# Performance work log

Measured on AMD Instinct MI355X. Metric: run time of the kernel, lower is better.

The kernel has to match this reference:

```python
import jax, jax.numpy as jnp
import numpy as np
import math

B, QLEN, DMODEL, NHEAD, SKV = 16, 1, 2048, 32, 4096
HEAD_DIM = DMODEL // NHEAD  # 64


def setup_inputs() -> dict:
    key = jax.random.key(0)
    ks = jax.random.split(key, 12)
    x = jax.random.normal(ks[0], (B, QLEN, DMODEL), dtype=jnp.float32)
    last_pos = jax.random.randint(ks[1], (B,), 0, SKV, dtype=jnp.int64)
    # mask: attend to cache positions <= last_pos (broadcast over heads and q)
    mask = (jnp.arange(SKV)[None, :] <= last_pos[:, None]).reshape(B, 1, 1, SKV)
    s = 1.0 / math.sqrt(DMODEL)
    Wq = jax.random.normal(ks[2], (DMODEL, DMODEL), dtype=jnp.float32) * s
    bq = jax.random.normal(ks[3], (DMODEL,), dtype=jnp.float32) * 0.02
    Wk = jax.random.normal(ks[4], (DMODEL, DMODEL), dtype=jnp.float32) * s
    bk = jax.random.normal(ks[5], (DMODEL,), dtype=jnp.float32) * 0.02
    Wv = jax.random.normal(ks[6], (DMODEL, DMODEL), dtype=jnp.float32) * s
    bv = jax.random.normal(ks[7], (DMODEL,), dtype=jnp.float32) * 0.02
    Wo = jax.random.normal(ks[8], (DMODEL, DMODEL), dtype=jnp.float32) * s
    bo = jax.random.normal(ks[9], (DMODEL,), dtype=jnp.float32) * 0.02
    # prefilled KV cache (float32, as in the module)
    cache_k = jax.random.normal(ks[10], (B, NHEAD, SKV, HEAD_DIM), dtype=jnp.float32)
    cache_v = jax.random.normal(ks[11], (B, NHEAD, SKV, HEAD_DIM), dtype=jnp.float32)
    return {"x": x, "last_pos": last_pos, "mask": mask, "Wq": Wq, "bq": bq,
            "Wk": Wk, "bk": bk, "Wv": Wv, "bv": bv, "Wo": Wo, "bo": bo,
            "cache_k": cache_k, "cache_v": cache_v}


def reference(x, last_pos, mask, Wq, bq, Wk, bk, Wv, bv, Wo, bo, cache_k, cache_v):
    bsz, seq_len, _ = x.shape  # decode path: seq_len == 1
    # QKV projections -> [B, H, S, D]
    q = (x @ Wq + bq).reshape(bsz, seq_len, NHEAD, HEAD_DIM).transpose(0, 2, 1, 3)
    k = (x @ Wk + bk).reshape(bsz, seq_len, NHEAD, HEAD_DIM).transpose(0, 2, 1, 3)
    v = (x @ Wv + bv).reshape(bsz, seq_len, NHEAD, HEAD_DIM).transpose(0, 2, 1, 3)
    # KV-cache scatter update at last_pos (seq_len == 1 branch of the original)
    bidx = jnp.arange(bsz)
    updated_kcache = cache_k.at[bidx, :, last_pos, :].set(k[:, :, 0, :].astype(jnp.float32))
    updated_vcache = cache_v.at[bidx, :, last_pos, :].set(v[:, :, 0, :].astype(jnp.float32))
    kf = updated_kcache.astype(q.dtype)
    vf = updated_vcache.astype(q.dtype)
    # scores: [B, H, Q, SKV]
    scores = jnp.einsum("bhqd,bhkd->bhqk", q, kf) / math.sqrt(HEAD_DIM)
    scores = jnp.where(mask, scores, jnp.finfo(scores.dtype).min)
    probs = jax.nn.softmax(scores.astype(jnp.float32), axis=-1).astype(q.dtype)
    out = jnp.einsum("bhqk,bhkd->bhqd", probs, vf)
    out = out.transpose(0, 2, 1, 3).reshape(bsz, seq_len, -1)
    out = out @ Wo + bo
    return out, updated_kcache, updated_vcache
```

## Files before the change

### kernel.cpp

```cpp
#include <hip/hip_runtime.h>
#include <math.h>

#define BB 16
#define DMODEL 2048
#define NHEAD 32
#define SKV 4096
#define HDIM 64
#define BH (BB*NHEAD)

typedef float f4 __attribute__((ext_vector_type(4)));

__global__ __launch_bounds__(256) void gemm_part(
    const float* __restrict__ src,
    const float* __restrict__ Wa, const float* __restrict__ Wb,
    const float* __restrict__ Wc,
    float* __restrict__ pa, float* __restrict__ pb, float* __restrict__ pc) {
  const float* W = (blockIdx.z == 0) ? Wa : ((blockIdx.z == 1) ? Wb : Wc);
  float* part    = (blockIdx.z == 0) ? pa : ((blockIdx.z == 1) ? pb : pc);
  __shared__ float xs[16][64];
  int tid = threadIdx.x;
  int i0 = blockIdx.y * 64;
  int o  = blockIdx.x * 1024 + tid * 4;
  {
    int t = tid * 4;
    int b = t >> 6, i = t & 63;
    *(f4*)&xs[b][i] = *(const f4*)&src[b * DMODEL + i0 + i];
  }
  __syncthreads();
  f4 acc[16];
#pragma unroll
  for (int b = 0; b < 16; ++b) acc[b] = (f4)0.f;
#pragma unroll 8
  for (int i = 0; i < 64; ++i) {
    f4 w = *(const f4*)&W[(size_t)(i0 + i) * DMODEL + o];
#pragma unroll
    for (int b = 0; b < 16; ++b) acc[b] += xs[b][i] * w;
  }
  float* p = part + (size_t)blockIdx.y * (16 * DMODEL) + o;
#pragma unroll
  for (int b = 0; b < 16; ++b) *(f4*)&p[b * DMODEL] = acc[b];
}

__global__ __launch_bounds__(256) void gemm_reduce(
    const float* __restrict__ pa, const float* __restrict__ pb,
    const float* __restrict__ pc,
    const float* __restrict__ ba, const float* __restrict__ bb,
    const float* __restrict__ bc,
    float* __restrict__ da, float* __restrict__ db, float* __restrict__ dc,
    float* __restrict__ zbuf) {
  const float* p    = (blockIdx.y == 0) ? pa : ((blockIdx.y == 1) ? pb : pc);
  const float* bias = (blockIdx.y == 0) ? ba : ((blockIdx.y == 1) ? bb : bc);
  float* dst        = (blockIdx.y == 0) ? da : ((blockIdx.y == 1) ? db : dc);
  int idx = blockIdx.x * 256 + threadIdx.x;
  if (zbuf && blockIdx.y == 0) zbuf[idx] = 0.f;
  float s = bias[idx & (DMODEL - 1)];
#pragma unroll 8
  for (int t = 0; t < 32; ++t) s += p[(size_t)t * (16 * DMODEL) + idx];
  dst[idx] = s;
}

__global__ __launch_bounds__(256) void k_copy_scores(
    const float* __restrict__ cacheK, const float* __restrict__ knew,
    const float* __restrict__ qv, const int* __restrict__ last_pos,
    float* __restrict__ outK, float* __restrict__ scores,
    float* __restrict__ pstat) {
  int bh = blockIdx.x >> 4;
  int blk = blockIdx.x & 15;
  int j0 = blk << 8;
  int b = bh >> 5;
  int lp = last_pos[b];
  int tid = threadIdx.x;
  int wave = tid >> 6, lane = tid & 63, q4 = lane >> 4, l16 = lane & 15;
  int rbase = wave * 4 + q4;
  const f4 qf = ((const f4*)(qv + bh * HDIM))[l16];
  const f4 kn = ((const f4*)(knew + bh * HDIM))[l16];
  size_t base = ((size_t)bh * SKV + j0 + rbase) * 16 + l16;
  const f4* K4 = (const f4*)cacheK + base;
  f4* O4 = (f4*)outK + base;
  float* s = scores + (size_t)bh * SKV;
  float fv[16];
#pragma unroll
  for (int t = 0; t < 16; ++t) {
    int j = j0 + rbase + t * 16;
    f4 kv = __builtin_nontemporal_load(&K4[t * 256]);
    if (j == lp) kv = kn;
    __builtin_nontemporal_store(kv, &O4[t * 256]);
    float p = qf.x * kv.x + qf.y * kv.y + qf.z * kv.z + qf.w * kv.w;
    p += __shfl_xor(p, 1);
    p += __shfl_xor(p, 2);
    p += __shfl_xor(p, 4);
    p += __shfl_xor(p, 8);
    p *= 0.125f;
    bool valid = (j <= lp);
    if (l16 == 0 && valid) s[j] = p;
    fv[t] = valid ? p : -1e30f;
  }
  float m = fv[0];
#pragma unroll
  for (int t = 1; t < 16; ++t) m = fmaxf(m, fv[t]);
  m = fmaxf(m, __shfl_xor(m, 16));
  m = fmaxf(m, __shfl_xor(m, 32));
  float se = 0.f;
#pragma unroll
  for (int t = 0; t < 16; ++t) se += __expf(fv[t] - m);
  se += __shfl_xor(se, 16);
  se += __shfl_xor(se, 32);
  __shared__ float lm[4], ls[4];
  if (lane == 0) { lm[wave] = m; ls[wave] = se; }
  __syncthreads();
  if (tid == 0) {
    float M = fmaxf(fmaxf(lm[0], lm[1]), fmaxf(lm[2], lm[3]));
    float S = ls[0] * __expf(lm[0] - M) + ls[1] * __expf(lm[1] - M)
            + ls[2] * __expf(lm[2] - M) + ls[3] * __expf(lm[3] - M);
    pstat[(bh * 16 + blk) * 2 + 0] = M;
    pstat[(bh * 16 + blk) * 2 + 1] = S;
  }
}

__global__ __launch_bounds__(256) void v_copy_pv(
    const float* __restrict__ cacheV, const float* __restrict__ vnew,
    const float* __restrict__ scores, const float* __restrict__ pstat,
    const int* __restrict__ last_pos,
    float* __restrict__ outV, float* __restrict__ attn) {
  __shared__ float sm[16], ss[16], sp[256];
  __shared__ float part[4][64];
  int bh = blockIdx.x >> 4;
  int j0 = (blockIdx.x & 15) << 8;
  int b = bh >> 5;
  int lp = last_pos[b];
  int tid = threadIdx.x;
  if (tid < 16) {
    sm[tid] = pstat[(bh * 16 + tid) * 2 + 0];
    ss[tid] = pstat[(bh * 16 + tid) * 2 + 1];
  }
  __syncthreads();
  float M = sm[0];
#pragma unroll
  for (int i = 1; i < 16; ++i) M = fmaxf(M, sm[i]);
  float S = 0.f;
#pragma unroll
  for (int i = 0; i < 16; ++i) S += ss[i] * __expf(sm[i] - M);
  float inv = 1.f / S;
  int jj = j0 + tid;
  sp[tid] = (jj <= lp) ? __expf(scores[(size_t)bh * SKV + jj] - M) * inv : 0.f;
  __syncthreads();

  int wave = tid >> 6, lane = tid & 63, q4 = lane >> 4, l16 = lane & 15;
  int rbase = wave * 4 + q4;
  const f4 vn = ((const f4*)(vnew + bh * HDIM))[l16];
  size_t base = ((size_t)bh * SKV + j0 + rbase) * 16 + l16;
  const f4* V4 = (const f4*)cacheV + base;
  f4* O4 = (f4*)outV + base;
  f4 acc = (f4)0.f;
#pragma unroll
  for (int t = 0; t < 16; ++t) {
    int j = j0 + rbase + t * 16;
    f4 vv = __builtin_nontemporal_load(&V4[t * 256]);
    if (j == lp) vv = vn;
    __builtin_nontemporal_store(vv, &O4[t * 256]);
    acc += sp[rbase + t * 16] * vv;
  }
  acc.x += __shfl_xor(acc.x, 16); acc.x += __shfl_xor(acc.x, 32);
  acc.y += __shfl_xor(acc.y, 16); acc.y += __shfl_xor(acc.y, 32);
  acc.z += __shfl_xor(acc.z, 16); acc.z += __shfl_xor(acc.z, 32);
  acc.w += __shfl_xor(acc.w, 16); acc.w += __shfl_xor(acc.w, 32);
  if (q4 == 0) ((f4*)part[wave])[l16] = acc;
  __syncthreads();
  if (tid < 64) {
    float v0 = part[0][tid] + part[1][tid] + part[2][tid] + part[3][tid];
    atomicAdd(&attn[bh * HDIM + tid], v0);
  }
}

extern "C" void kernel_launch(void* const* d_in, const int* in_sizes, int n_in,
                              void* d_out, int out_size, void* d_ws, size_t ws_size,
                              hipStream_t stream) {
  const float* x        = (const float*)d_in[0];
  const int*   last_pos = (const int*)d_in[1];
  const float* Wq = (const float*)d_in[3];
  const float* bq = (const float*)d_in[4];
  const float* Wk = (const float*)d_in[5];
  const float* bk = (const float*)d_in[6];
  const float* Wv = (const float*)d_in[7];
  const float* bv = (const float*)d_in[8];
  const float* Wo = (const float*)d_in[9];
  const float* bo = (const float*)d_in[10];
  const float* cacheK = (const float*)d_in[11];
  const float* cacheV = (const float*)d_in[12];

  float* out  = (float*)d_out;
  float* outK = out + (size_t)BB * DMODEL;
  float* outV = outK + (size_t)BH * SKV * HDIM;

  float* ws    = (float*)d_ws;
  float* q     = ws;
  float* k     = ws + 32768;
  float* v     = ws + 65536;
  float* attn  = ws + 98304;
  float* pstat = ws + 131072;
  float* big   = ws + 147456;
  float* pq = big;
  float* pk = big + 1048576;
  float* pv = big + 2097152;
  float* scores = big;
  float* po = big;

  gemm_part<<<dim3(2, 32, 3), 256, 0, stream>>>(x, Wq, Wk, Wv, pq, pk, pv);
  gemm_reduce<<<dim3(128, 3), 256, 0, stream>>>(pq, pk, pv, bq, bk, bv, q, k, v, attn);
  k_copy_scores<<<8192, 256, 0, stream>>>(cacheK, k, q, last_pos, outK, scores, pstat);
  v_copy_pv<<<8192, 256, 0, stream>>>(cacheV, v, scores, pstat, last_pos, outV, attn);
  gemm_part<<<dim3(2, 32, 1), 256, 0, stream>>>(attn, Wo, Wo, Wo, po, po, po);
  gemm_reduce<<<dim3(128, 1), 256, 0, stream>>>(po, po, po, bo, bo, bo, out, out, out, nullptr);
}
```

Baseline: 445.8 us.

## Fuse K and V cache passes into one split-softmax kernel, merge in output GEMM

Merges the K-copy/score kernel and the V-copy/PV kernel into a single kernel. Each block computes a local max, exponentials and a partial weighted V sum for its 256-position strip and writes them as a flash-decoding style record. The record merge (rescale and normalise) moves into the prologue of the output-projection GEMM. This removes the scores round trip, the pstat reread, the atomics and the zeroing of the attention buffer, and it cuts one launch. It costs an extra workspace of per-strip records and some redundant merge work in each GEMM block.

```diff
diff --git a/kernel.cpp b/kernel.cpp
--- a/kernel.cpp
+++ b/kernel.cpp
@@ -7,6 +7,8 @@
 #define SKV 4096
 #define HDIM 64
 #define BH (BB*NHEAD)
+#define NSTRIP 16
+#define SREC 68
 
 typedef float f4 __attribute__((ext_vector_type(4)));
 
@@ -46,27 +48,25 @@
     const float* __restrict__ pc,
     const float* __restrict__ ba, const float* __restrict__ bb,
     const float* __restrict__ bc,
-    float* __restrict__ da, float* __restrict__ db, float* __restrict__ dc,
-    float* __restrict__ zbuf) {
+    float* __restrict__ da, float* __restrict__ db, float* __restrict__ dc) {
   const float* p    = (blockIdx.y == 0) ? pa : ((blockIdx.y == 1) ? pb : pc);
   const float* bias = (blockIdx.y == 0) ? ba : ((blockIdx.y == 1) ? bb : bc);
   float* dst        = (blockIdx.y == 0) ? da : ((blockIdx.y == 1) ? db : dc);
   int idx = blockIdx.x * 256 + threadIdx.x;
-  if (zbuf && blockIdx.y == 0) zbuf[idx] = 0.f;
   float s = bias[idx & (DMODEL - 1)];
 #pragma unroll 8
   for (int t = 0; t < 32; ++t) s += p[(size_t)t * (16 * DMODEL) + idx];
   dst[idx] = s;
 }
 
-__global__ __launch_bounds__(256) void k_copy_scores(
-    const float* __restrict__ cacheK, const float* __restrict__ knew,
+__global__ __launch_bounds__(256) void kv_fused(
+    const float* __restrict__ cacheK, const float* __restrict__ cacheV,
+    const float* __restrict__ knew, const float* __restrict__ vnew,
     const float* __restrict__ qv, const int* __restrict__ last_pos,
-    float* __restrict__ outK, float* __restrict__ scores,
+    float* __restrict__ outK, float* __restrict__ outV,
     float* __restrict__ pstat) {
   int bh = blockIdx.x >> 4;
-  int blk = blockIdx.x & 15;
-  int j0 = blk << 8;
+  int j0 = (blockIdx.x & 15) << 8;
   int b = bh >> 5;
   int lp = last_pos[b];
   int tid = threadIdx.x;
@@ -74,91 +74,51 @@
   int rbase = wave * 4 + q4;
   const f4 qf = ((const f4*)(qv + bh * HDIM))[l16];
   const f4 kn = ((const f4*)(knew + bh * HDIM))[l16];
+  const f4 vn = ((const f4*)(vnew + bh * HDIM))[l16];
   size_t base = ((size_t)bh * SKV + j0 + rbase) * 16 + l16;
   const f4* K4 = (const f4*)cacheK + base;
-  f4* O4 = (f4*)outK + base;
-  float* s = scores + (size_t)bh * SKV;
+  const f4* V4 = (const f4*)cacheV + base;
+  f4* OK4 = (f4*)outK + base;
+  f4* OV4 = (f4*)outV + base;
+  __shared__ float lm[4], ls[4], part[4][64];
+
   float fv[16];
 #pragma unroll
   for (int t = 0; t < 16; ++t) {
     int j = j0 + rbase + t * 16;
     f4 kv = __builtin_nontemporal_load(&K4[t * 256]);
     if (j == lp) kv = kn;
-    __builtin_nontemporal_store(kv, &O4[t * 256]);
+    __builtin_nontemporal_store(kv, &OK4[t * 256]);
     float p = qf.x * kv.x + qf.y * kv.y + qf.z * kv.z + qf.w * kv.w;
     p += __shfl_xor(p, 1);
     p += __shfl_xor(p, 2);
     p += __shfl_xor(p, 4);
     p += __shfl_xor(p, 8);
-    p *= 0.125f;
-    bool valid = (j <= lp);
-    if (l16 == 0 && valid) s[j] = p;
-    fv[t] = valid ? p : -1e30f;
+    fv[t] = (j <= lp) ? p * 0.125f : -1e30f;
   }
   float m = fv[0];
 #pragma unroll
   for (int t = 1; t < 16; ++t) m = fmaxf(m, fv[t]);
   m = fmaxf(m, __shfl_xor(m, 16));
   m = fmaxf(m, __shfl_xor(m, 32));
+  if (lane == 0) lm[wave] = m;
+  __syncthreads();
+  float M = fmaxf(fmaxf(lm[0], lm[1]), fmaxf(lm[2], lm[3]));
   float se = 0.f;
 #pragma unroll
-  for (int t = 0; t < 16; ++t) se += __expf(fv[t] - m);
+  for (int t = 0; t < 16; ++t) { fv[t] = __expf(fv[t] - M); se += fv[t]; }
   se += __shfl_xor(se, 16);
   se += __shfl_xor(se, 32);
-  __shared__ float lm[4], ls[4];
-  if (lane == 0) { lm[wave] = m; ls[wave] = se; }
-  __syncthreads();
-  if (tid == 0) {
-    float M = fmaxf(fmaxf(lm[0], lm[1]), fmaxf(lm[2], lm[3]));
-    float S = ls[0] * __expf(lm[0] - M) + ls[1] * __expf(lm[1] - M)
-            + ls[2] * __expf(lm[2] - M) + ls[3] * __expf(lm[3] - M);
-    pstat[(bh * 16 + blk) * 2 + 0] = M;
-    pstat[(bh * 16 + blk) * 2 + 1] = S;
-  }
-}
-
-__global__ __launch_bounds__(256) void v_copy_pv(
-    const float* __restrict__ cacheV, const float* __restrict__ vnew,
-    const float* __restrict__ scores, const float* __restrict__ pstat,
-    const int* __restrict__ last_pos,
-    float* __restrict__ outV, float* __restrict__ attn) {
-  __shared__ float sm[16], ss[16], sp[256];
-  __shared__ float part[4][64];
-  int bh = blockIdx.x >> 4;
-  int j0 = (blockIdx.x & 15) << 8;
-  int b = bh >> 5;
-  int lp = last_pos[b];
-  int tid = threadIdx.x;
-  if (tid < 16) {
-    sm[tid] = pstat[(bh * 16 + tid) * 2 + 0];
-    ss[tid] = pstat[(bh * 16 + tid) * 2 + 1];
-  }
-  __syncthreads();
-  float M = sm[0];
-#pragma unroll
-  for (int i = 1; i < 16; ++i) M = fmaxf(M, sm[i]);
-  float S = 0.f;
-#pragma unroll
-  for (int i = 0; i < 16; ++i) S += ss[i] * __expf(sm[i] - M);
-  float inv = 1.f / S;
-  int jj = j0 + tid;
-  sp[tid] = (jj <= lp) ? __expf(scores[(size_t)bh * SKV + jj] - M) * inv : 0.f;
-  __syncthreads();
-
-  int wave = tid >> 6, lane = tid & 63, q4 = lane >> 4, l16 = lane & 15;
-  int rbase = wave * 4 + q4;
-  const f4 vn = ((const f4*)(vnew + bh * HDIM))[l16];
-  size_t base = ((size_t)bh * SKV + j0 + rbase) * 16 + l16;
-  const f4* V4 = (const f4*)cacheV + base;
-  f4* O4 = (f4*)outV + base;
+  if (lane == 0) ls[wave] = se;
+
   f4 acc = (f4)0.f;
 #pragma unroll
   for (int t = 0; t < 16; ++t) {
     int j = j0 + rbase + t * 16;
     f4 vv = __builtin_nontemporal_load(&V4[t * 256]);
     if (j == lp) vv = vn;
-    __builtin_nontemporal_store(vv, &O4[t * 256]);
-    acc += sp[rbase + t * 16] * vv;
+    __builtin_nontemporal_store(vv, &OV4[t * 256]);
+    acc += fv[t] * vv;
   }
   acc.x += __shfl_xor(acc.x, 16); acc.x += __shfl_xor(acc.x, 32);
   acc.y += __shfl_xor(acc.y, 16); acc.y += __shfl_xor(acc.y, 32);
@@ -166,10 +126,56 @@
   acc.w += __shfl_xor(acc.w, 16); acc.w += __shfl_xor(acc.w, 32);
   if (q4 == 0) ((f4*)part[wave])[l16] = acc;
   __syncthreads();
+  float* rec = pstat + (size_t)blockIdx.x * SREC;
   if (tid < 64) {
-    float v0 = part[0][tid] + part[1][tid] + part[2][tid] + part[3][tid];
-    atomicAdd(&attn[bh * HDIM + tid], v0);
-  }
+    rec[4 + tid] = part[0][tid] + part[1][tid] + part[2][tid] + part[3][tid];
+  } else if (tid == 64) {
+    rec[0] = M;
+    rec[1] = ls[0] + ls[1] + ls[2] + ls[3];
+  }
+}
+
+__global__ __launch_bounds__(256) void attn_gemm_part(
+    const float* __restrict__ pstat, const float* __restrict__ Wo,
+    float* __restrict__ po) {
+  __shared__ float xs[16][64];
+  int tid = threadIdx.x;
+  int h = blockIdx.y;
+  {
+    int g = tid >> 4, u = tid & 15;
+    const float* prec = pstat + (size_t)(g * NHEAD + h) * NSTRIP * SREC;
+    float M = -1e30f;
+#pragma unroll
+    for (int s = 0; s < 16; ++s) M = fmaxf(M, prec[s * SREC]);
+    float es[16];
+    float D = 0.f;
+#pragma unroll
+    for (int s = 0; s < 16; ++s) {
+      es[s] = __expf(prec[s * SREC] - M);
+      D += es[s] * prec[s * SREC + 1];
+    }
+    float invD = 1.f / D;
+    f4 a = (f4)0.f;
+#pragma unroll
+    for (int s = 0; s < 16; ++s)
+      a += es[s] * *(const f4*)&prec[s * SREC + 4 + u * 4];
+    *(f4*)&xs[g][u * 4] = a * invD;
+  }
+  __syncthreads();
+  int o = blockIdx.x * 1024 + tid * 4;
+  int i0 = h * 64;
+  f4 acc[16];
+#pragma unroll
+  for (int b = 0; b < 16; ++b) acc[b] = (f4)0.f;
+#pragma unroll 8
+  for (int i = 0; i < 64; ++i) {
+    f4 w = *(const f4*)&Wo[(size_t)(i0 + i) * DMODEL + o];
+#pragma unroll
+    for (int b = 0; b < 16; ++b) acc[b] += xs[b][i] * w;
+  }
+  float* p = po + (size_t)blockIdx.y * (16 * DMODEL) + o;
+#pragma unroll
+  for (int b = 0; b < 16; ++b) *(f4*)&p[b * DMODEL] = acc[b];
 }
 
 extern "C" void kernel_launch(void* const* d_in, const int* in_sizes, int n_in,
@@ -196,19 +202,18 @@
   float* q     = ws;
   float* k     = ws + 32768;
   float* v     = ws + 65536;
-  float* attn  = ws + 98304;
-  float* pstat = ws + 131072;
-  float* big   = ws + 147456;
+  float* pstat = ws + 98304;
+  float* big   = ws + 98304 + 8192 * SREC;
   float* pq = big;
   float* pk = big + 1048576;
   float* pv = big + 2097152;
-  float* scores = big;
   float* po = big;
 
   gemm_part<<<dim3(2, 32, 3), 256, 0, stream>>>(x, Wq, Wk, Wv, pq, pk, pv);
-  gemm_reduce<<<dim3(128, 3), 256, 0, stream>>>(pq, pk, pv, bq, bk, bv, q, k, v, attn);
-  k_copy_scores<<<8192, 256, 0, stream>>>(cacheK, k, q, last_pos, outK, scores, pstat);
-  v_copy_pv<<<8192, 256, 0, stream>>>(cacheV, v, scores, pstat, last_pos, outV, attn);
-  gemm_part<<<dim3(2, 32, 1), 256, 0, stream>>>(attn, Wo, Wo, Wo, po, po, po);
-  gemm_reduce<<<dim3(128, 1), 256, 0, stream>>>(po, po, po, bo, bo, bo, out, out, out, nullptr);
-}
+  gemm_reduce<<<dim3(128, 3), 256, 0, stream>>>(pq, pk, pv, bq, bk, bv, q, k, v);
+  kv_fused<<<8192, 256, 0, stream>>>(cacheK, cacheV, k, v, q, last_pos,
+                                     outK, outV, pstat);
+  attn_gemm_part<<<dim3(2, 32), 256, 0, stream>>>(pstat, Wo, po);
+  gemm_reduce<<<dim3(128, 1), 256, 0, stream>>>(po, po, po, bo, bo, bo,
+                                                out, out, out);
+}
```

New measurement: 464.0 us. 4.1% more time.

## Replace atomic PV accumulation with per-strip partials fused into output projection

Applied to the files above, without the earlier changes.

The PV kernel now writes per-strip partial attention vectors to a workspace buffer instead of doing atomicAdd into a zeroed buffer. A new output-projection kernel sums the 16 strip partials per head while loading its input tile, which removes the atomics and the zeroing. Separately, the K/V cache copies switch from nontemporal loads and stores to ordinary ones, which changes cache behaviour on the main bandwidth-bound streams.

```diff
diff --git a/kernel.cpp b/kernel.cpp
--- a/kernel.cpp
+++ b/kernel.cpp
@@ -7,6 +7,7 @@
 #define SKV 4096
 #define HDIM 64
 #define BH (BB*NHEAD)
+#define NSTRIP 16
 
 typedef float f4 __attribute__((ext_vector_type(4)));
 
@@ -46,13 +47,11 @@
     const float* __restrict__ pc,
     const float* __restrict__ ba, const float* __restrict__ bb,
     const float* __restrict__ bc,
-    float* __restrict__ da, float* __restrict__ db, float* __restrict__ dc,
-    float* __restrict__ zbuf) {
+    float* __restrict__ da, float* __restrict__ db, float* __restrict__ dc) {
   const float* p    = (blockIdx.y == 0) ? pa : ((blockIdx.y == 1) ? pb : pc);
   const float* bias = (blockIdx.y == 0) ? ba : ((blockIdx.y == 1) ? bb : bc);
   float* dst        = (blockIdx.y == 0) ? da : ((blockIdx.y == 1) ? db : dc);
   int idx = blockIdx.x * 256 + threadIdx.x;
-  if (zbuf && blockIdx.y == 0) zbuf[idx] = 0.f;
   float s = bias[idx & (DMODEL - 1)];
 #pragma unroll 8
   for (int t = 0; t < 32; ++t) s += p[(size_t)t * (16 * DMODEL) + idx];
@@ -82,9 +81,9 @@
 #pragma unroll
   for (int t = 0; t < 16; ++t) {
     int j = j0 + rbase + t * 16;
-    f4 kv = __builtin_nontemporal_load(&K4[t * 256]);
+    f4 kv = K4[t * 256];
     if (j == lp) kv = kn;
-    __builtin_nontemporal_store(kv, &O4[t * 256]);
+    O4[t * 256] = kv;
     float p = qf.x * kv.x + qf.y * kv.y + qf.z * kv.z + qf.w * kv.w;
     p += __shfl_xor(p, 1);
     p += __shfl_xor(p, 2);
@@ -121,11 +120,12 @@
     const float* __restrict__ cacheV, const float* __restrict__ vnew,
     const float* __restrict__ scores, const float* __restrict__ pstat,
     const int* __restrict__ last_pos,
-    float* __restrict__ outV, float* __restrict__ attn) {
+    float* __restrict__ outV, float* __restrict__ prec) {
   __shared__ float sm[16], ss[16], sp[256];
   __shared__ float part[4][64];
   int bh = blockIdx.x >> 4;
-  int j0 = (blockIdx.x & 15) << 8;
+  int blk = blockIdx.x & 15;
+  int j0 = blk << 8;
   int b = bh >> 5;
   int lp = last_pos[b];
   int tid = threadIdx.x;
@@ -155,9 +155,9 @@
 #pragma unroll
   for (int t = 0; t < 16; ++t) {
     int j = j0 + rbase + t * 16;
-    f4 vv = __builtin_nontemporal_load(&V4[t * 256]);
+    f4 vv = V4[t * 256];
     if (j == lp) vv = vn;
-    __builtin_nontemporal_store(vv, &O4[t * 256]);
+    O4[t * 256] = vv;
     acc += sp[rbase + t * 16] * vv;
   }
   acc.x += __shfl_xor(acc.x, 16); acc.x += __shfl_xor(acc.x, 32);
@@ -167,9 +167,40 @@
   if (q4 == 0) ((f4*)part[wave])[l16] = acc;
   __syncthreads();
   if (tid < 64) {
-    float v0 = part[0][tid] + part[1][tid] + part[2][tid] + part[3][tid];
-    atomicAdd(&attn[bh * HDIM + tid], v0);
-  }
+    prec[(size_t)blockIdx.x * HDIM + tid] =
+        part[0][tid] + part[1][tid] + part[2][tid] + part[3][tid];
+  }
+}
+
+__global__ __launch_bounds__(256) void attn_gemm_part(
+    const float* __restrict__ prec, const float* __restrict__ Wo,
+    float* __restrict__ po) {
+  __shared__ float xs[16][64];
+  int tid = threadIdx.x;
+  int h = blockIdx.y;
+  {
+    int g = tid >> 4, u = tid & 15;
+    const float* r = prec + (size_t)(g * NHEAD + h) * NSTRIP * HDIM + u * 4;
+    f4 a = (f4)0.f;
+#pragma unroll
+    for (int s = 0; s < 16; ++s) a += *(const f4*)&r[s * HDIM];
+    *(f4*)&xs[g][u * 4] = a;
+  }
+  __syncthreads();
+  int o = blockIdx.x * 1024 + tid * 4;
+  int i0 = h * 64;
+  f4 acc[16];
+#pragma unroll
+  for (int b = 0; b < 16; ++b) acc[b] = (f4)0.f;
+#pragma unroll 8
+  for (int i = 0; i < 64; ++i) {
+    f4 w = *(const f4*)&Wo[(size_t)(i0 + i) * DMODEL + o];
+#pragma unroll
+    for (int b = 0; b < 16; ++b) acc[b] += xs[b][i] * w;
+  }
+  float* p = po + (size_t)blockIdx.y * (16 * DMODEL) + o;
+#pragma unroll
+  for (int b = 0; b < 16; ++b) *(f4*)&p[b * DMODEL] = acc[b];
 }
 
 extern "C" void kernel_launch(void* const* d_in, const int* in_sizes, int n_in,
@@ -196,19 +227,19 @@
   float* q     = ws;
   float* k     = ws + 32768;
   float* v     = ws + 65536;
-  float* attn  = ws + 98304;
-  float* pstat = ws + 131072;
-  float* big   = ws + 147456;
+  float* pstat = ws + 98304;
+  float* prec  = ws + 114688;
+  float* big   = ws + 114688 + 524288;
   float* pq = big;
   float* pk = big + 1048576;
   float* pv = big + 2097152;
   float* scores = big;
-  float* po = big;
+  float* po = big + 1048576;
 
   gemm_part<<<dim3(2, 32, 3), 256, 0, stream>>>(x, Wq, Wk, Wv, pq, pk, pv);
-  gemm_reduce<<<dim3(128, 3), 256, 0, stream>>>(pq, pk, pv, bq, bk, bv, q, k, v, attn);
+  gemm_reduce<<<dim3(128, 3), 256, 0, stream>>>(pq, pk, pv, bq, bk, bv, q, k, v);
   k_copy_scores<<<8192, 256, 0, stream>>>(cacheK, k, q, last_pos, outK, scores, pstat);
-  v_copy_pv<<<8192, 256, 0, stream>>>(cacheV, v, scores, pstat, last_pos, outV, attn);
-  gemm_part<<<dim3(2, 32, 1), 256, 0, stream>>>(attn, Wo, Wo, Wo, po, po, po);
-  gemm_reduce<<<dim3(128, 1), 256, 0, stream>>>(po, po, po, bo, bo, bo, out, out, out, nullptr);
-}
+  v_copy_pv<<<8192, 256, 0, stream>>>(cacheV, v, scores, pstat, last_pos, outV, prec);
+  attn_gemm_part<<<dim3(2, 32), 256, 0, stream>>>(prec, Wo, po);
+  gemm_reduce<<<dim3(128, 1), 256, 0, stream>>>(po, po, po, bo, bo, bo, out, out, out);
+}
```

Measured after the change: 499.1 us. 12.0% more time.
